# Optimization experiments

Measured on AMD Instinct MI355X. Metric: run time of the kernel, lower is better.

## Reference

```python
import jax, jax.numpy as jnp
import numpy as np

EPS = 1e-7
B, N, DIM, NH, HD, WIN, HASH_WIN = 2, 1024, 512, 8, 64, 64, 8


def expmap0(v, c):
    sqrt_c = jnp.clip(jnp.sqrt(c), EPS)
    v_norm = jnp.linalg.norm(v, axis=-1, keepdims=True)
    is_zero = v_norm < EPS
    safe = jnp.clip(v_norm, EPS)
    mag = jnp.tanh(sqrt_c * safe) / sqrt_c
    return jnp.where(is_zero, jnp.zeros_like(v), mag * (v / safe))


def poincare_dist(x, y, c):
    # x: (B,H,N,1,D), y: (B,H,N,W,D), c: (B,1,1,1,1) -> (B,H,N,W)
    sqrt_c = jnp.clip(jnp.sqrt(c), EPS)
    x2 = jnp.sum(x * x, -1, keepdims=True)
    y2 = jnp.sum(y * y, -1, keepdims=True)
    xy = jnp.sum(x * y, -1, keepdims=True)
    num = (1 - 2 * c * xy + c * y2) * x + (1 - c * x2) * (-y)
    den = 1 - 2 * c * xy + c * c * x2 * y2
    diff = num / jnp.clip(den, EPS)
    dn = jnp.linalg.norm(diff, axis=-1)
    arg = jnp.minimum(jnp.squeeze(sqrt_c, -1) * jnp.clip(dn, EPS), 1.0 - EPS)
    return 2.0 * jnp.arctanh(arg) / jnp.squeeze(sqrt_c, -1)


def sliding_windows(t, w):
    # t: (B,H,N,D) -> (B,H,N,w,D), left-padded causal window
    Bb, H, Nn, D = t.shape
    pad = jnp.zeros((Bb, H, w - 1, D), t.dtype)
    tp = jnp.concatenate([pad, t], axis=2)
    idx = jnp.arange(w)[None, :] + jnp.arange(Nn)[:, None]  # (N,w)
    return tp[:, :, idx, :]


def layernorm(x, s, b):
    m = jnp.mean(x, -1, keepdims=True)
    v = jnp.var(x, -1, keepdims=True)
    return (x - m) / jnp.sqrt(v + 1e-6) * s + b


def rope(x, cos, sin):
    # x: (B,N,H,hd), cos/sin: (N, hd//2) -- complex rotation in real arithmetic
    xr, xi = jnp.split(x, 2, axis=-1)
    cos = cos[None, :, None, :]
    sin = sin[None, :, None, :]
    return jnp.concatenate([xr * cos - xi * sin, xr * sin + xi * cos], axis=-1)


def setup_inputs() -> dict:
    key = jax.random.key(0)
    ks = jax.random.split(key, 10)
    x = jax.random.normal(ks[0], (B, N, DIM), jnp.float32)
    pos = jnp.arange(N, dtype=jnp.float32)
    inv = 1.0 / (10000.0 ** (jnp.arange(0, HD, 2, dtype=jnp.float32) / HD))
    ang = pos[:, None] * inv[None, :]  # (N, HD//2)
    freqs_cos, freqs_sin = jnp.cos(ang), jnp.sin(ang)
    c = jax.random.uniform(ks[1], (B,), jnp.float32) * 0.9 + 0.1
    s = 0.02
    Wq = jax.random.normal(ks[2], (DIM, DIM), jnp.float32) * s
    Wk = jax.random.normal(ks[3], (DIM, DIM), jnp.float32) * s
    Wv = jax.random.normal(ks[4], (DIM, DIM), jnp.float32) * s
    Wo = jax.random.normal(ks[5], (DIM, DIM), jnp.float32) * s
    W1 = jax.random.normal(ks[6], (DIM, 4 * DIM), jnp.float32) * s
    W2 = jax.random.normal(ks[7], (4 * DIM, DIM), jnp.float32) * s
    bq = jnp.zeros((DIM,)); bk = jnp.zeros((DIM,)); bv = jnp.zeros((DIM,))
    bo = jnp.zeros((DIM,)); b1 = jnp.zeros((4 * DIM,)); b2 = jnp.zeros((DIM,))
    ln1_s = jnp.ones((DIM,)); ln1_b = jnp.zeros((DIM,))
    ln2_s = jnp.ones((DIM,)); ln2_b = jnp.zeros((DIM,))
    geo_scale = jnp.ones((NH, 1, 1), jnp.float32)
    hash_offset = jax.random.normal(ks[8], (1, 1, NH, HD), jnp.float32) * 0.01
    return dict(x=x, freqs_cos=freqs_cos, freqs_sin=freqs_sin, c=c,
                Wq=Wq, bq=bq, Wk=Wk, bk=bk, Wv=Wv, bv=bv, Wo=Wo, bo=bo,
                W1=W1, b1=b1, W2=W2, b2=b2,
                ln1_s=ln1_s, ln1_b=ln1_b, ln2_s=ln2_s, ln2_b=ln2_b,
                geo_scale=geo_scale, hash_offset=hash_offset)


def reference(x, freqs_cos, freqs_sin, c, Wq, bq, Wk, bk, Wv, bv, Wo, bo,
              W1, b1, W2, b2, ln1_s, ln1_b, ln2_s, ln2_b, geo_scale, hash_offset):
    x_res = x
    xn = layernorm(x, ln1_s, ln1_b)
    q = (xn @ Wq + bq).reshape(B, N, NH, HD)
    k = (xn @ Wk + bk).reshape(B, N, NH, HD)
    v = (xn @ Wv + bv).reshape(B, N, NH, HD)
    q = q + hash_offset * jnp.log(1.0 + HASH_WIN)
    q_rot = rope(q, freqs_cos, freqs_sin)
    k_rot = rope(k, freqs_cos, freqs_sin)
    c_b = c.reshape(B, 1, 1, 1)
    q_h = expmap0(q_rot, c_b)
    k_h = expmap0(k_rot, c_b)
    q_h, k_h, v = (t.transpose(0, 2, 1, 3) for t in (q_h, k_h, v))  # (B,H,N,D)
    k_win = sliding_windows(k_h, WIN)  # (B,H,N,W,D)
    v_win = sliding_windows(v, WIN)
    dist = poincare_dist(q_h[:, :, :, None, :], k_win, c.reshape(B, 1, 1, 1, 1))  # (B,H,N,W)
    scores = -geo_scale * dist
    w = jax.nn.softmax(scores, axis=-1)
    attn = jnp.einsum('bhnw,bhnwd->bhnd', w, v_win)
    attn = attn.transpose(0, 2, 1, 3).reshape(B, N, DIM)
    x_out = x_res + (attn @ Wo + bo)
    h = layernorm(x_out, ln2_s, ln2_b)
    ffn = jax.nn.gelu(h @ W1 + b1) @ W2 + b2
    return x_out + ffn
```

## Files before the change

### kernel.cpp

```cpp
#include <hip/hip_runtime.h>
#include <math.h>
#include <stdint.h>

#define Bn   2
#define Nn   1024
#define DIMn 512
#define NHn  8
#define HDn  64
#define QKVS 1536
#define EPSF 1e-7f

typedef __attribute__((ext_vector_type(8))) short short8;
typedef __attribute__((ext_vector_type(4))) float floatx4;

__device__ __forceinline__ unsigned short f2bf(float f) {
  union { float f; uint32_t u; } v; v.f = f;
  uint32_t u = v.u;
  return (unsigned short)((u + 0x7FFFu + ((u >> 16) & 1u)) >> 16);
}
__device__ __forceinline__ float bf2f(unsigned short h) {
  union { uint32_t u; float f; } v; v.u = ((uint32_t)h) << 16;
  return v.f;
}

__device__ __forceinline__ float wsum(float v) {
#pragma unroll
  for (int m = 32; m >= 1; m >>= 1) v += __shfl_xor(v, m, 64);
  return v;
}
__device__ __forceinline__ float wmax(float v) {
#pragma unroll
  for (int m = 32; m >= 1; m >>= 1) v = fmaxf(v, __shfl_xor(v, m, 64));
  return v;
}

__device__ __forceinline__ float gelu_tanh(float x) {
  const float k0 = 0.7978845608028654f;
  float x3 = x * x * x;
  return 0.5f * x * (1.f + tanhf(k0 * (x + 0.044715f * x3)));
}

__device__ __forceinline__ void glds16(const unsigned short* g, unsigned short* l) {
  __builtin_amdgcn_global_load_lds((const __attribute__((address_space(1))) void*)g,
                                   (__attribute__((address_space(3))) void*)l, 16, 0, 0);
}

__global__ __launch_bounds__(256) void prep_kernel(
    const float* __restrict__ Wq, const float* __restrict__ Wk,
    const float* __restrict__ Wv, const float* __restrict__ Wo,
    const float* __restrict__ W1, const float* __restrict__ W2,
    unsigned short* __restrict__ Wcat_hi, unsigned short* __restrict__ Wcat_lo,
    unsigned short* __restrict__ Wo_t, unsigned short* __restrict__ W1_t,
    unsigned short* __restrict__ W2_t,
    const float* __restrict__ bq, const float* __restrict__ bk,
    const float* __restrict__ bv, float* __restrict__ bias_cat,
    const float* __restrict__ x, const float* __restrict__ ln1s,
    const float* __restrict__ ln1b,
    unsigned short* __restrict__ xn_hi, unsigned short* __restrict__ xn_lo) {
  __shared__ float t[32][33];
  __shared__ float red[2][4];
  int bid = blockIdx.x;
  int tid = threadIdx.x;
  if (bid == 3072) {
    for (int i = tid; i < 512; i += 256) {
      bias_cat[i] = bq[i];
      bias_cat[512 + i] = bk[i];
      bias_cat[1024 + i] = bv[i];
    }
    return;
  }
  if (bid > 3072) {
    int row = bid - 3073;
    const float* xr = x + (size_t)row * DIMn;
    float2 xv = *(const float2*)(xr + tid * 2);
    float s  = xv.x + xv.y;
    float s2 = xv.x * xv.x + xv.y * xv.y;
    s = wsum(s); s2 = wsum(s2);
    int wv = tid >> 6;
    if ((tid & 63) == 0) { red[0][wv] = s; red[1][wv] = s2; }
    __syncthreads();
    s  = red[0][0] + red[0][1] + red[0][2] + red[0][3];
    s2 = red[1][0] + red[1][1] + red[1][2] + red[1][3];
    float mean = s * (1.f / DIMn);
    float var  = s2 * (1.f / DIMn) - mean * mean;
    float rstd = rsqrtf(var + 1e-6f);
    int d = tid * 2;
    float2 gv = *(const float2*)(ln1s + d);
    float2 bv2 = *(const float2*)(ln1b + d);
    float o0 = (xv.x - mean) * rstd * gv.x + bv2.x;
    float o1 = (xv.y - mean) * rstd * gv.y + bv2.y;
    size_t idx = (size_t)row * DIMn + d;
    unsigned short h0 = f2bf(o0), h1 = f2bf(o1);
    ushort2 hv; hv.x = h0; hv.y = h1;
    *(ushort2*)(xn_hi + idx) = hv;
    ushort2 lv; lv.x = f2bf(o0 - bf2f(h0)); lv.y = f2bf(o1 - bf2f(h1));
    *(ushort2*)(xn_lo + idx) = lv;
    return;
  }
  const float* W;
  unsigned short* hi;
  unsigned short* lo = nullptr;
  int K, N, tix;
  if (bid < 256)       { W = Wq; hi = Wcat_hi;               lo = Wcat_lo;               K = 512;  N = 512;  tix = bid; }
  else if (bid < 512)  { W = Wk; hi = Wcat_hi + 512 * 512;   lo = Wcat_lo + 512 * 512;   K = 512;  N = 512;  tix = bid - 256; }
  else if (bid < 768)  { W = Wv; hi = Wcat_hi + 1024 * 512;  K = 512;  N = 512;  tix = bid - 512; }
  else if (bid < 1024) { W = Wo; hi = Wo_t;                  K = 512;  N = 512;  tix = bid - 768; }
  else if (bid < 2048) { W = W1; hi = W1_t;                  K = 512;  N = 2048; tix = bid - 1024; }
  else                 { W = W2; hi = W2_t;                  K = 2048; N = 512;  tix = bid - 2048; }
  int ntn = N >> 5;
  int kt = tix / ntn, nt = tix - kt * ntn;
  int k0 = kt * 32, n0 = nt * 32;
  for (int i = tid; i < 1024; i += 256) {
    int r = i >> 5, c = i & 31;
    t[r][c] = W[(size_t)(k0 + r) * N + n0 + c];
  }
  __syncthreads();
  for (int i = tid; i < 1024; i += 256) {
    int r = i >> 5, c = i & 31;
    float v = t[c][r];
    unsigned short h = f2bf(v);
    size_t oi = (size_t)(n0 + r) * K + k0 + c;
    hi[oi] = h;
    if (lo) lo[oi] = f2bf(v - bf2f(h));
  }
}

template <int BM, int BN, int BKT, int SPLIT, int EPI, int OUTBF16>
__global__ __launch_bounds__(256) void gemm_mfma(
    const unsigned short* __restrict__ Ahi, const unsigned short* __restrict__ Alo,
    const unsigned short* __restrict__ Bhi, const unsigned short* __restrict__ Blo,
    const float* __restrict__ bias, const float* __restrict__ res,
    void* __restrict__ outp, int M, int N, int K) {
  constexpr int FI = BM / 32, FJ = BN / 32;
  constexpr int AE = BM * BKT, BE = BN * BKT;
  constexpr int NB = (SPLIT > 0) ? 2 : 1;
  constexpr int CPR = BKT / 8;
  constexpr int ACH = BM * CPR, BCH = BN * CPR;
  __shared__ unsigned short smem[NB * (AE + BE)];
  unsigned short* AsHi = smem;
  unsigned short* AsLo = smem + ((SPLIT > 0) ? AE : 0);
  unsigned short* BsHi = smem + NB * AE;
  unsigned short* BsLo = BsHi + ((SPLIT > 0) ? BE : 0);

  int tid = threadIdx.x;
  int lane = tid & 63;
  int wid = tid >> 6;
  int wm = (wid >> 1) * (BM / 2), wn = (wid & 1) * (BN / 2);
  int bm = blockIdx.y * BM, bn = blockIdx.x * BN;
  int m16 = lane & 15, kg = lane >> 4;
  bool dos = (SPLIT == 1) || (SPLIT == 2 && bn < 1024);

  floatx4 acc[FI][FJ];
#pragma unroll
  for (int i = 0; i < FI; ++i)
#pragma unroll
    for (int j = 0; j < FJ; ++j) { floatx4 z = {0.f, 0.f, 0.f, 0.f}; acc[i][j] = z; }

  const unsigned short* aph = Ahi + (size_t)bm * K;
  const unsigned short* bph = Bhi + (size_t)bn * K;
  const unsigned short* apl = (SPLIT > 0) ? (Alo + (size_t)bm * K) : nullptr;
  const unsigned short* bpl = (SPLIT > 0) ? (Blo + (size_t)bn * K) : nullptr;

  for (int k0 = 0; k0 < K; k0 += BKT) {
#pragma unroll
    for (int c = tid; c < ACH; c += 256) {
      int row = c / CPR, kk = (c % CPR) * 8;
      glds16(aph + (size_t)row * K + k0 + kk, AsHi + c * 8);
      if (SPLIT > 0 && dos) glds16(apl + (size_t)row * K + k0 + kk, AsLo + c * 8);
    }
#pragma unroll
    for (int c = tid; c < BCH; c += 256) {
      int row = c / CPR, kk = (c % CPR) * 8;
      glds16(bph + (size_t)row * K + k0 + kk, BsHi + c * 8);
      if (SPLIT > 0 && dos) glds16(bpl + (size_t)row * K + k0 + kk, BsLo + c * 8);
    }
    __syncthreads();

#pragma unroll
    for (int ks = 0; ks < BKT / 32; ++ks) {
      short8 ah[FI], bh[FJ];
      short8 al[(SPLIT > 0) ? FI : 1], bl[(SPLIT > 0) ? FJ : 1];
#pragma unroll
      for (int i = 0; i < FI; ++i) {
        int r = wm + i * 16 + m16;
        ah[i] = *(const short8*)&AsHi[r * BKT + ks * 32 + kg * 8];
        if (SPLIT > 0 && dos) al[i] = *(const short8*)&AsLo[r * BKT + ks * 32 + kg * 8];
      }
#pragma unroll
      for (int j = 0; j < FJ; ++j) {
        int r = wn + j * 16 + m16;
        bh[j] = *(const short8*)&BsHi[r * BKT + ks * 32 + kg * 8];
        if (SPLIT > 0 && dos) bl[j] = *(const short8*)&BsLo[r * BKT + ks * 32 + kg * 8];
      }
#pragma unroll
      for (int i = 0; i < FI; ++i)
#pragma unroll
        for (int j = 0; j < FJ; ++j) {
          acc[i][j] = __builtin_amdgcn_mfma_f32_16x16x32_bf16(ah[i], bh[j], acc[i][j], 0, 0, 0);
          if (SPLIT > 0) {
            if (dos) {
              acc[i][j] = __builtin_amdgcn_mfma_f32_16x16x32_bf16(al[i], bh[j], acc[i][j], 0, 0, 0);
              acc[i][j] = __builtin_amdgcn_mfma_f32_16x16x32_bf16(ah[i], bl[j], acc[i][j], 0, 0, 0);
            }
          }
        }
    }
    __syncthreads();
  }

#pragma unroll
  for (int i = 0; i < FI; ++i) {
    int gr0 = bm + wm + i * 16 + kg * 4;
#pragma unroll
    for (int j = 0; j < FJ; ++j) {
      int gc = bn + wn + j * 16 + m16;
      float bsv = bias[gc];
#pragma unroll
      for (int r = 0; r < 4; ++r) {
        size_t idx = (size_t)(gr0 + r) * N + gc;
        float v = acc[i][j][r] + bsv;
        if constexpr (EPI == 1) v += res[idx];
        if constexpr (EPI == 2) v = gelu_tanh(v);
        if constexpr (OUTBF16) ((unsigned short*)outp)[idx] = f2bf(v);
        else ((float*)outp)[idx] = v;
      }
    }
  }
}

__global__ __launch_bounds__(256) void ffn1_ln(
    const float* __restrict__ xout, const float* __restrict__ g,
    const float* __restrict__ be,
    const unsigned short* __restrict__ W1t, const float* __restrict__ b1,
    unsigned short* __restrict__ mid) {
  constexpr int BM = 64, BN = 128, BK = 64;
  constexpr int AST = BK + 8;
  __shared__ unsigned short As[BM * AST];
  __shared__ unsigned short Bs[BN * BK];
  __shared__ float mrs[BM][2];

  int tid = threadIdx.x, lane = tid & 63, wid = tid >> 6;
  int bm = blockIdx.y * BM, bn = blockIdx.x * BN;
  int m16 = lane & 15, kg = lane >> 4;
  int wm = (wid >> 1) * (BM / 2), wn = (wid & 1) * (BN / 2);

#pragma unroll 4
  for (int i = 0; i < 16; ++i) {
    int row = wid * 16 + i;
    const float* xr = xout + (size_t)(bm + row) * DIMn;
    float4 a = ((const float4*)xr)[lane * 2];
    float4 b = ((const float4*)xr)[lane * 2 + 1];
    float s  = a.x + a.y + a.z + a.w + b.x + b.y + b.z + b.w;
    float s2 = a.x*a.x + a.y*a.y + a.z*a.z + a.w*a.w + b.x*b.x + b.y*b.y + b.z*b.z + b.w*b.w;
    s = wsum(s); s2 = wsum(s2);
    if (lane == 0) {
      float mean = s * (1.f / DIMn);
      float var  = s2 * (1.f / DIMn) - mean * mean;
      mrs[row][0] = mean;
      mrs[row][1] = rsqrtf(var + 1e-6f);
    }
  }
  __syncthreads();

  floatx4 acc[2][4];
#pragma unroll
  for (int i = 0; i < 2; ++i)
#pragma unroll
    for (int j = 0; j < 4; ++j) { floatx4 z = {0.f, 0.f, 0.f, 0.f}; acc[i][j] = z; }

  for (int k0 = 0; k0 < DIMn; k0 += BK) {
    {
      int row = tid >> 2, c0 = (tid & 3) * 16;
      const float* xr = xout + (size_t)(bm + row) * DIMn + k0 + c0;
      float mean = mrs[row][0], rstd = mrs[row][1];
      unsigned short* dst = &As[row * AST + c0];
#pragma unroll
      for (int j = 0; j < 2; ++j) {
        float4 v0 = ((const float4*)xr)[j * 2];
        float4 v1 = ((const float4*)xr)[j * 2 + 1];
        float4 g0 = ((const float4*)(g + k0 + c0))[j * 2];
        float4 g1 = ((const float4*)(g + k0 + c0))[j * 2 + 1];
        float4 e0 = ((const float4*)(be + k0 + c0))[j * 2];
        float4 e1 = ((const float4*)(be + k0 + c0))[j * 2 + 1];
        short8 o;
        o[0] = (short)f2bf((v0.x - mean) * rstd * g0.x + e0.x);
        o[1] = (short)f2bf((v0.y - mean) * rstd * g0.y + e0.y);
        o[2] = (short)f2bf((v0.z - mean) * rstd * g0.z + e0.z);
        o[3] = (short)f2bf((v0.w - mean) * rstd * g0.w + e0.w);
        o[4] = (short)f2bf((v1.x - mean) * rstd * g1.x + e1.x);
        o[5] = (short)f2bf((v1.y - mean) * rstd * g1.y + e1.y);
        o[6] = (short)f2bf((v1.z - mean) * rstd * g1.z + e1.z);
        o[7] = (short)f2bf((v1.w - mean) * rstd * g1.w + e1.w);
        *(short8*)(dst + j * 8) = o;
      }
    }
#pragma unroll
    for (int c = tid; c < BN * 8; c += 256) {
      int row = c >> 3, kk = (c & 7) * 8;
      glds16(W1t + (size_t)(bn + row) * DIMn + k0 + kk, Bs + c * 8);
    }
    __syncthreads();

#pragma unroll
    for (int ks = 0; ks < 2; ++ks) {
      short8 ah[2], bh[4];
#pragma unroll
      for (int i = 0; i < 2; ++i)
        ah[i] = *(const short8*)&As[(wm + i * 16 + m16) * AST + ks * 32 + kg * 8];
#pragma unroll
      for (int j = 0; j < 4; ++j)
        bh[j] = *(const short8*)&Bs[(wn + j * 16 + m16) * BK + ks * 32 + kg * 8];
#pragma unroll
      for (int i = 0; i < 2; ++i)
#pragma unroll
        for (int j = 0; j < 4; ++j)
          acc[i][j] = __builtin_amdgcn_mfma_f32_16x16x32_bf16(ah[i], bh[j], acc[i][j], 0, 0, 0);
    }
    __syncthreads();
  }

#pragma unroll
  for (int i = 0; i < 2; ++i) {
    int gr0 = bm + wm + i * 16 + kg * 4;
#pragma unroll
    for (int j = 0; j < 4; ++j) {
      int gc = bn + wn + j * 16 + m16;
      float bsv = b1[gc];
#pragma unroll
      for (int r = 0; r < 4; ++r) {
        float v = gelu_tanh(acc[i][j][r] + bsv);
        mid[(size_t)(gr0 + r) * 2048 + gc] = f2bf(v);
      }
    }
  }
}

__global__ __launch_bounds__(512) void attn_fused(const float* __restrict__ qkv,
                                                  const float* __restrict__ fcos,
                                                  const float* __restrict__ fsin,
                                                  const float* __restrict__ cvec,
                                                  const float* __restrict__ geo,
                                                  const float* __restrict__ hash,
                                                  unsigned short* __restrict__ attn_out) {
  __shared__ unsigned short Qhi[32][72], Qlo[32][72];
  __shared__ unsigned short Khi[96][72], Klo[96][72];
  __shared__ unsigned short Vt[64][104];
  __shared__ unsigned short Pb[32][104];
  __shared__ float Sf[32][97];
  __shared__ float x2s[32], bxs[32], y2s[96], gys[96];

  int tid = threadIdx.x, lane = tid & 63, wv = tid >> 6;
  int bid = blockIdx.x;
  int nt = bid & 31, h = (bid >> 5) & 7, b = bid >> 8;
  int n0 = nt * 32;
  float c = cvec[b];
  float sqc = sqrtf(c);
  float rsqc = 1.f / sqc;
  float gs = geo[h];
  int dr = lane & 31;
  bool hih = lane >= 32;
  const float LOG9 = 2.1972245773362196f;
  float hofr = hash[h * HDn + dr] * LOG9;
  float hofi = hash[h * HDn + dr + 32] * LOG9;

  for (int i = tid; i < 32 * 52; i += 512) ((uint32_t*)Pb)[i] = 0u;

#pragma unroll
  for (int i = 0; i < 4; ++i) {
    int q = wv * 4 + i;
    int n = n0 + q;
    size_t bas = (size_t)(b * Nn + n) * QKVS + h * HDn;
    float qr = qkv[bas + dr] + hofr;
    float qi = qkv[bas + dr + 32] + hofi;
    float cs = fcos[n * 32 + dr], sn = fsin[n * 32 + dr];
    float qv = hih ? (qr * sn + qi * cs) : (qr * cs - qi * sn);
    float nq = sqrtf(wsum(qv * qv));
    float sq = fmaxf(nq, EPSF);
    float t = sqc * sq;
    float em = expf(-2.f * t);
    float opem = 1.f + em;
    float mag = ((1.f - em) / opem) * rsqc;
    float sech2 = 4.f * em / (opem * opem);
    float oq = (nq < EPSF) ? 0.f : mag * (qv / sq);
    unsigned short hh = f2bf(oq);
    Qhi[q][lane] = hh;
    Qlo[q][lane] = f2bf(oq - bf2f(hh));
    if (lane == 0) {
      x2s[q] = (nq < EPSF) ? 0.f : mag * mag;
      bxs[q] = (nq < EPSF) ? 1.f : sech2;
    }
  }
#pragma unroll 4
  for (int i = 0; i < 12; ++i) {
    int r = wv * 12 + i;
    int gi = n0 - 64 + r;
    float ok = 0.f, vf = 0.f, y2 = 0.f, gy = 1.f;
    if (gi >= 0) {
      size_t bas = (size_t)(b * Nn + gi) * QKVS + h * HDn;
      float kr = qkv[bas + 512 + dr];
      float ki = qkv[bas + 512 + dr + 32];
      vf = qkv[bas + 1024 + lane];
      float cs = fcos[gi * 32 + dr], sn = fsin[gi * 32 + dr];
      float kv = hih ? (kr * sn + ki * cs) : (kr * cs - ki * sn);
      float nk = sqrtf(wsum(kv * kv));
      float sk = fmaxf(nk, EPSF);
      float t = sqc * sk;
      float em = expf(-2.f * t);
      float opem = 1.f + em;
      float mag = ((1.f - em) / opem) * rsqc;
      float sech2 = 4.f * em / (opem * opem);
      ok = (nk < EPSF) ? 0.f : mag * (kv / sk);
      y2 = (nk < EPSF) ? 0.f : mag * mag;
      gy = (nk < EPSF) ? 1.f : sech2;
    }
    unsigned short hh = f2bf(ok);
    Khi[r][lane] = hh;
    Klo[r][lane] = f2bf(ok - bf2f(hh));
    Vt[lane][r] = f2bf(vf);
    if (lane == 0) { y2s[r] = y2; gys[r] = gy; }
  }
  __syncthreads();

  int m16 = lane & 15, kg = lane >> 4;
#pragma unroll
  for (int uu = 0; uu < 2; ++uu) {
    int u = wv + uu * 8;
    if (u < 12) {
      int mt = u / 6, ntile = u % 6;
      floatx4 acc = {0.f, 0.f, 0.f, 0.f};
#pragma unroll
      for (int ks = 0; ks < 2; ++ks) {
        short8 ah = *(const short8*)&Qhi[mt * 16 + m16][ks * 32 + kg * 8];
        short8 al = *(const short8*)&Qlo[mt * 16 + m16][ks * 32 + kg * 8];
        short8 bh = *(const short8*)&Khi[ntile * 16 + m16][ks * 32 + kg * 8];
        short8 bl = *(const short8*)&Klo[ntile * 16 + m16][ks * 32 + kg * 8];
        acc = __builtin_amdgcn_mfma_f32_16x16x32_bf16(ah, bh, acc, 0, 0, 0);
        acc = __builtin_amdgcn_mfma_f32_16x16x32_bf16(al, bh, acc, 0, 0, 0);
        acc = __builtin_amdgcn_mfma_f32_16x16x32_bf16(ah, bl, acc, 0, 0, 0);
      }
#pragma unroll
      for (int r = 0; r < 4; ++r) Sf[mt * 16 + kg * 4 + r][ntile * 16 + m16] = acc[r];
    }
  }
  __syncthreads();

#pragma unroll
  for (int i = 0; i < 4; ++i) {
    int nl = wv * 4 + i;
    int r = nl + 1 + lane;
    float xy = Sf[nl][r];
    float x2 = x2s[nl], y2 = y2s[r];
    float bx = bxs[nl], gy = gys[r];

    float den = fmaf(c * c * x2, y2, fmaf(-2.f * c, xy, 1.f));
    den = fmaxf(den, EPSF);
    float rden = 1.f / den;
    float s2 = fmaxf(x2 - 2.f * xy + y2, 0.f);
    float z = sqrtf(c * s2 * rden);
    float omz2 = bx * gy * rden;
    float opz = 1.f + fminf(z, 1.f);
    float ratio = fminf(opz * opz / omz2, 1.9999999e7f);
    float sc = -gs * logf(ratio) * rsqc;

    float mx = wmax(sc);
    float e = expf(sc - mx);
    float se = wsum(e);
    Pb[nl][r] = f2bf(e / se);
  }
  __syncthreads();

  {
    int mt = wv >> 2, ntile = wv & 3;
    floatx4 acc = {0.f, 0.f, 0.f, 0.f};
#pragma unroll
    for (int ks = 0; ks < 3; ++ks) {
      short8 a = *(const short8*)&Pb[mt * 16 + m16][ks * 32 + kg * 8];
      short8 bb = *(const short8*)&Vt[ntile * 16 + m16][ks * 32 + kg * 8];
      acc = __builtin_amdgcn_mfma_f32_16x16x32_bf16(a, bb, acc, 0, 0, 0);
    }
#pragma unroll
    for (int r = 0; r < 4; ++r) {
      int qrow = mt * 16 + kg * 4 + r;
      int d = ntile * 16 + m16;
      attn_out[(size_t)(b * Nn + n0 + qrow) * DIMn + h * HDn + d] = f2bf(acc[r]);
    }
  }
}

extern "C" void kernel_launch(void* const* d_in, const int* in_sizes, int n_in,
                              void* d_out, int out_size, void* d_ws, size_t ws_size,
                              hipStream_t stream) {
  const float* x    = (const float*)d_in[0];
  const float* fcos = (const float*)d_in[1];
  const float* fsin = (const float*)d_in[2];
  const float* cvec = (const float*)d_in[3];
  const float* Wq = (const float*)d_in[4];  const float* bq = (const float*)d_in[5];
  const float* Wk = (const float*)d_in[6];  const float* bk = (const float*)d_in[7];
  const float* Wv = (const float*)d_in[8];  const float* bv = (const float*)d_in[9];
  const float* Wo = (const float*)d_in[10]; const float* bo = (const float*)d_in[11];
  const float* W1 = (const float*)d_in[12]; const float* b1 = (const float*)d_in[13];
  const float* W2 = (const float*)d_in[14]; const float* b2 = (const float*)d_in[15];
  const float* ln1s = (const float*)d_in[16]; const float* ln1b = (const float*)d_in[17];
  const float* ln2s = (const float*)d_in[18]; const float* ln2b = (const float*)d_in[19];
  const float* geo  = (const float*)d_in[20]; const float* hash = (const float*)d_in[21];
  float* out = (float*)d_out;
  char* base = (char*)d_ws;

  unsigned short* Wcat_hi = (unsigned short*)(base + 0);
  unsigned short* Wcat_lo = (unsigned short*)(base + 1572864);
  unsigned short* Wo_t    = (unsigned short*)(base + 3145728);
  unsigned short* W1_t    = (unsigned short*)(base + 3670016);
  unsigned short* W2_t    = (unsigned short*)(base + 5767168);
  unsigned short* xn_hi   = (unsigned short*)(base + 7864320);
  unsigned short* xn_lo   = (unsigned short*)(base + 9961472);
  float*          qkv     = (float*)(base + 12058624);
  unsigned short* attnb   = (unsigned short*)(base + 7864320);
  float*          xout    = (float*)(base + 9961472);
  unsigned short* mid     = (unsigned short*)(base + 16252928);
  float*          bias_cat= (float*)(base + 24641536);

  const int M = Bn * Nn;

  prep_kernel<<<3073 + M, 256, 0, stream>>>(Wq, Wk, Wv, Wo, W1, W2, Wcat_hi, Wcat_lo,
                                            Wo_t, W1_t, W2_t, bq, bk, bv, bias_cat,
                                            x, ln1s, ln1b, xn_hi, xn_lo);
  gemm_mfma<64, 64, 32, 2, 0, 0><<<dim3(QKVS / 64, M / 64), 256, 0, stream>>>(
      xn_hi, xn_lo, Wcat_hi, Wcat_lo, bias_cat, nullptr, qkv, M, QKVS, 512);
  attn_fused<<<Bn * NHn * (Nn / 32), 512, 0, stream>>>(qkv, fcos, fsin, cvec, geo, hash, attnb);
  gemm_mfma<32, 64, 128, 0, 1, 0><<<dim3(DIMn / 64, M / 32), 256, 0, stream>>>(
      attnb, nullptr, Wo_t, nullptr, bo, x, xout, M, DIMn, 512);
  ffn1_ln<<<dim3(2048 / 128, M / 64), 256, 0, stream>>>(
      xout, ln2s, ln2b, W1_t, b1, mid);
  gemm_mfma<32, 64, 128, 0, 1, 0><<<dim3(DIMn / 64, M / 32), 256, 0, stream>>>(
      mid, nullptr, W2_t, nullptr, b2, xout, out, M, DIMn, 2048);
}
```

Baseline: 215.4 us.

## Stage full normalized A rows once in ffn1_ln with smaller M tile

The fused LayerNorm+FFN1 kernel now uses a 32-row M tile and normalizes the whole 32x512 A block into shared memory once before the K loop, rather than renormalizing a 64-wide slice every iteration. This doubles the grid along M for more parallelism and takes normalization work and its sync dependency out of the K loop. Each wave now does one MFMA row-tile instead of two, which halves A-fragment reuse. The Wo and W2 GEMMs also switch to a smaller K tile (128 to 64).

```diff
diff --git a/kernel.cpp b/kernel.cpp
--- a/kernel.cpp
+++ b/kernel.cpp
@@ -233,8 +233,8 @@
     const float* __restrict__ be,
     const unsigned short* __restrict__ W1t, const float* __restrict__ b1,
     unsigned short* __restrict__ mid) {
-  constexpr int BM = 64, BN = 128, BK = 64;
-  constexpr int AST = BK + 8;
+  constexpr int BM = 32, BN = 128, BK = 64;
+  constexpr int AST = 512 + 8;
   __shared__ unsigned short As[BM * AST];
   __shared__ unsigned short Bs[BN * BK];
   __shared__ float mrs[BM][2];
@@ -242,11 +242,11 @@
   int tid = threadIdx.x, lane = tid & 63, wid = tid >> 6;
   int bm = blockIdx.y * BM, bn = blockIdx.x * BN;
   int m16 = lane & 15, kg = lane >> 4;
-  int wm = (wid >> 1) * (BM / 2), wn = (wid & 1) * (BN / 2);
-
-#pragma unroll 4
-  for (int i = 0; i < 16; ++i) {
-    int row = wid * 16 + i;
+  int wm = (wid >> 1) * 16, wn = (wid & 1) * 64;
+
+#pragma unroll
+  for (int i = 0; i < 8; ++i) {
+    int row = wid * 8 + i;
     const float* xr = xout + (size_t)(bm + row) * DIMn;
     float4 a = ((const float4*)xr)[lane * 2];
     float4 b = ((const float4*)xr)[lane * 2 + 1];
@@ -262,38 +262,37 @@
   }
   __syncthreads();
 
-  floatx4 acc[2][4];
-#pragma unroll
-  for (int i = 0; i < 2; ++i)
-#pragma unroll
-    for (int j = 0; j < 4; ++j) { floatx4 z = {0.f, 0.f, 0.f, 0.f}; acc[i][j] = z; }
+  {
+    int row = tid >> 3, c0 = (tid & 7) * 64;
+    float mean = mrs[row][0], rstd = mrs[row][1];
+    const float* xr = xout + (size_t)(bm + row) * DIMn + c0;
+    unsigned short* dst = &As[row * AST + c0];
+#pragma unroll
+    for (int j = 0; j < 8; ++j) {
+      float4 v0 = ((const float4*)xr)[j * 2];
+      float4 v1 = ((const float4*)xr)[j * 2 + 1];
+      float4 g0 = ((const float4*)(g + c0))[j * 2];
+      float4 g1 = ((const float4*)(g + c0))[j * 2 + 1];
+      float4 e0 = ((const float4*)(be + c0))[j * 2];
+      float4 e1 = ((const float4*)(be + c0))[j * 2 + 1];
+      short8 o;
+      o[0] = (short)f2bf((v0.x - mean) * rstd * g0.x + e0.x);
+      o[1] = (short)f2bf((v0.y - mean) * rstd * g0.y + e0.y);
+      o[2] = (short)f2bf((v0.z - mean) * rstd * g0.z + e0.z);
+      o[3] = (short)f2bf((v0.w - mean) * rstd * g0.w + e0.w);
+      o[4] = (short)f2bf((v1.x - mean) * rstd * g1.x + e1.x);
+      o[5] = (short)f2bf((v1.y - mean) * rstd * g1.y + e1.y);
+      o[6] = (short)f2bf((v1.z - mean) * rstd * g1.z + e1.z);
+      o[7] = (short)f2bf((v1.w - mean) * rstd * g1.w + e1.w);
+      *(short8*)(dst + j * 8) = o;
+    }
+  }
+
+  floatx4 acc[4];
+#pragma unroll
+  for (int j = 0; j < 4; ++j) { floatx4 z = {0.f, 0.f, 0.f, 0.f}; acc[j] = z; }
 
   for (int k0 = 0; k0 < DIMn; k0 += BK) {
-    {
-      int row = tid >> 2, c0 = (tid & 3) * 16;
-      const float* xr = xout + (size_t)(bm + row) * DIMn + k0 + c0;
-      float mean = mrs[row][0], rstd = mrs[row][1];
-      unsigned short* dst = &As[row * AST + c0];
-#pragma unroll
-      for (int j = 0; j < 2; ++j) {
-        float4 v0 = ((const float4*)xr)[j * 2];
-        float4 v1 = ((const float4*)xr)[j * 2 + 1];
-        float4 g0 = ((const float4*)(g + k0 + c0))[j * 2];
-        float4 g1 = ((const float4*)(g + k0 + c0))[j * 2 + 1];
-        float4 e0 = ((const float4*)(be + k0 + c0))[j * 2];
-        float4 e1 = ((const float4*)(be + k0 + c0))[j * 2 + 1];
-        short8 o;
-        o[0] = (short)f2bf((v0.x - mean) * rstd * g0.x + e0.x);
-        o[1] = (short)f2bf((v0.y - mean) * rstd * g0.y + e0.y);
-        o[2] = (short)f2bf((v0.z - mean) * rstd * g0.z + e0.z);
-        o[3] = (short)f2bf((v0.w - mean) * rstd * g0.w + e0.w);
-        o[4] = (short)f2bf((v1.x - mean) * rstd * g1.x + e1.x);
-        o[5] = (short)f2bf((v1.y - mean) * rstd * g1.y + e1.y);
-        o[6] = (short)f2bf((v1.z - mean) * rstd * g1.z + e1.z);
-        o[7] = (short)f2bf((v1.w - mean) * rstd * g1.w + e1.w);
-        *(short8*)(dst + j * 8) = o;
-      }
-    }
 #pragma unroll
     for (int c = tid; c < BN * 8; c += 256) {
       int row = c >> 3, kk = (c & 7) * 8;
@@ -303,34 +302,27 @@
 
 #pragma unroll
     for (int ks = 0; ks < 2; ++ks) {
-      short8 ah[2], bh[4];
-#pragma unroll
-      for (int i = 0; i < 2; ++i)
-        ah[i] = *(const short8*)&As[(wm + i * 16 + m16) * AST + ks * 32 + kg * 8];
+      short8 ah = *(const short8*)&As[(wm + m16) * AST + k0 + ks * 32 + kg * 8];
+      short8 bh[4];
 #pragma unroll
       for (int j = 0; j < 4; ++j)
         bh[j] = *(const short8*)&Bs[(wn + j * 16 + m16) * BK + ks * 32 + kg * 8];
 #pragma unroll
-      for (int i = 0; i < 2; ++i)
-#pragma unroll
-        for (int j = 0; j < 4; ++j)
-          acc[i][j] = __builtin_amdgcn_mfma_f32_16x16x32_bf16(ah[i], bh[j], acc[i][j], 0, 0, 0);
+      for (int j = 0; j < 4; ++j)
+        acc[j] = __builtin_amdgcn_mfma_f32_16x16x32_bf16(ah, bh[j], acc[j], 0, 0, 0);
     }
     __syncthreads();
   }
 
-#pragma unroll
-  for (int i = 0; i < 2; ++i) {
-    int gr0 = bm + wm + i * 16 + kg * 4;
-#pragma unroll
-    for (int j = 0; j < 4; ++j) {
-      int gc = bn + wn + j * 16 + m16;
-      float bsv = b1[gc];
-#pragma unroll
-      for (int r = 0; r < 4; ++r) {
-        float v = gelu_tanh(acc[i][j][r] + bsv);
-        mid[(size_t)(gr0 + r) * 2048 + gc] = f2bf(v);
-      }
+  int gr0 = bm + wm + kg * 4;
+#pragma unroll
+  for (int j = 0; j < 4; ++j) {
+    int gc = bn + wn + j * 16 + m16;
+    float bsv = b1[gc];
+#pragma unroll
+    for (int r = 0; r < 4; ++r) {
+      float v = gelu_tanh(acc[j][r] + bsv);
+      mid[(size_t)(gr0 + r) * 2048 + gc] = f2bf(v);
     }
   }
 }
@@ -527,10 +519,10 @@
   gemm_mfma<64, 64, 32, 2, 0, 0><<<dim3(QKVS / 64, M / 64), 256, 0, stream>>>(
       xn_hi, xn_lo, Wcat_hi, Wcat_lo, bias_cat, nullptr, qkv, M, QKVS, 512);
   attn_fused<<<Bn * NHn * (Nn / 32), 512, 0, stream>>>(qkv, fcos, fsin, cvec, geo, hash, attnb);
-  gemm_mfma<32, 64, 128, 0, 1, 0><<<dim3(DIMn / 64, M / 32), 256, 0, stream>>>(
+  gemm_mfma<32, 64, 64, 0, 1, 0><<<dim3(DIMn / 64, M / 32), 256, 0, stream>>>(
       attnb, nullptr, Wo_t, nullptr, bo, x, xout, M, DIMn, 512);
-  ffn1_ln<<<dim3(2048 / 128, M / 64), 256, 0, stream>>>(
+  ffn1_ln<<<dim3(2048 / 128, M / 32), 256, 0, stream>>>(
       xout, ln2s, ln2b, W1_t, b1, mid);
-  gemm_mfma<32, 64, 128, 0, 1, 0><<<dim3(DIMn / 64, M / 32), 256, 0, stream>>>(
+  gemm_mfma<32, 64, 64, 0, 1, 0><<<dim3(DIMn / 64, M / 32), 256, 0, stream>>>(
       mid, nullptr, W2_t, nullptr, b2, xout, out, M, DIMn, 2048);
 }
```

After: 221.5 us. 2.8% more time.
